# Kernel optimization log

Measured on AMD Instinct MI355X. Metric: run time of the kernel, lower is better.

The kernel has to match this reference:

```python
import jax, jax.numpy as jnp
import numpy as np

N = 100000      # total nodes across the batch of graphs
E = 1600000     # total edges (avg degree 16)
D = 128         # dim_drug (== num_feature here)
L = 3           # layer_drug
G = 2048        # number of graphs in the batch
BN_EPS = 1e-5


def setup_inputs() -> dict:
    key = jax.random.key(0)
    ks = jax.random.split(key, 10)
    x = jax.random.normal(ks[0], (N, D), dtype=jnp.float32)
    edge_index = jax.random.randint(ks[1], (2, E), 0, N, dtype=jnp.int64)
    batch = jnp.sort(jax.random.randint(ks[2], (N,), 0, G, dtype=jnp.int64))
    s = 0.05
    W1 = jax.random.normal(ks[3], (L, D, D), dtype=jnp.float32) * s
    b1 = jax.random.normal(ks[4], (L, D), dtype=jnp.float32) * s
    W2 = jax.random.normal(ks[5], (L, D, D), dtype=jnp.float32) * s
    b2 = jax.random.normal(ks[6], (L, D), dtype=jnp.float32) * s
    gamma = jnp.ones((L, D), dtype=jnp.float32)
    beta = jnp.zeros((L, D), dtype=jnp.float32)
    return {"x": x, "edge_index": edge_index, "batch": batch,
            "W1": W1, "b1": b1, "W2": W2, "b2": b2,
            "gamma": gamma, "beta": beta}


def reference(x, edge_index, batch, W1, b1, W2, b2, gamma, beta):
    src, dst = edge_index[0], edge_index[1]
    h = x
    layer_outs = []
    for i in range(L):
        # GINConv, eps=0: MLP( (1+eps)*h + sum_{j->i} h_j )
        agg = jax.ops.segment_sum(h[src], dst, num_segments=N)  # [N, D]
        m = agg + h
        m = jax.nn.relu(m @ W1[i] + b1[i]) @ W2[i] + b2[i]       # 2-layer MLP
        m = jax.nn.relu(m)                                        # F.relu after conv
        # BatchNorm1d (training mode: batch stats over node dim, biased var)
        mean = jnp.mean(m, axis=0)
        var = jnp.mean((m - mean) ** 2, axis=0)
        h = gamma[i] * (m - mean) * jax.lax.rsqrt(var + BN_EPS) + beta[i]
        layer_outs.append(h)
    node_rep = jnp.concatenate(layer_outs, axis=1)  # JK 'cat' -> [N, L*D]
    return jax.ops.segment_max(node_rep, batch, num_segments=G)  # [G, L*D]
```

## Files before the change

kernel.cpp:

```cpp
#include <hip/hip_runtime.h>
#include <stdint.h>

#define NN 100000
#define NE 1600000
#define DD 128
#define NL 3
#define NG 2048
#define BN_EPS 1e-5f
#define CAP 56
#define GSH 9
#define GSZ 512
#define NGRP 196
#define GBINCAP 9216
#define MAXSEG 16

typedef short s16x8 __attribute__((ext_vector_type(8)));
typedef float f32x4 __attribute__((ext_vector_type(4)));

__device__ __forceinline__ unsigned short f2bfu(float f) {
    union { float f; unsigned int i; } x; x.f = f;
    unsigned int r = x.i + 0x7fffu + ((x.i >> 16) & 1u);
    return (unsigned short)(r >> 16);
}
__device__ __forceinline__ float bfu2f(unsigned short u) {
    union { unsigned int i; float f; } x; x.i = ((unsigned int)u) << 16; return x.f;
}
__device__ __forceinline__ float uplo(unsigned int u) {
    union { unsigned int i; float f; } x; x.i = u << 16; return x.f;
}
__device__ __forceinline__ float uphi(unsigned int u) {
    union { unsigned int i; float f; } x; x.i = u & 0xffff0000u; return x.f;
}
__device__ __forceinline__ void add8(float* a, uint4 v) {
    a[0] += uplo(v.x); a[1] += uphi(v.x);
    a[2] += uplo(v.y); a[3] += uphi(v.y);
    a[4] += uplo(v.z); a[5] += uphi(v.z);
    a[6] += uplo(v.w); a[7] += uphi(v.w);
}
__device__ __forceinline__ unsigned int pack2(float a, float b) {
    return (unsigned int)f2bfu(a) | ((unsigned int)f2bfu(b) << 16);
}

__global__ __launch_bounds__(256) void k_cvt(
    const float* __restrict__ x, unsigned short* __restrict__ hb)
{
    int i = (blockIdx.x * 256 + threadIdx.x) * 4;
    if (i >= NN * DD) return;
    float4 v = *(const float4*)(x + i);
    ushort4 o;
    o.x = f2bfu(v.x); o.y = f2bfu(v.y); o.z = f2bfu(v.z); o.w = f2bfu(v.w);
    *(ushort4*)(hb + i) = o;
}

__global__ __launch_bounds__(256) void k_wtrans(
    const float* __restrict__ W1, const float* __restrict__ W2,
    unsigned short* __restrict__ Wt)
{
    int idx = blockIdx.x * 256 + threadIdx.x;
    if (idx >= 6 * DD * DD) return;
    int mat = idx >> 14;
    int r = idx & 16383;
    int n = r >> 7, k = r & 127;
    const float* src = (mat < 3) ? (W1 + mat * DD * DD) : (W2 + (mat - 3) * DD * DD);
    Wt[idx] = f2bfu(src[k * DD + n]);
}

__global__ __launch_bounds__(256) void k_bounds(
    const int* __restrict__ batch, int* __restrict__ start)
{
    int n = blockIdx.x * 256 + threadIdx.x;
    if (n >= NN) return;
    int bn = batch[n];
    bn = bn < 0 ? 0 : (bn > NG - 1 ? NG - 1 : bn);
    int bp;
    if (n == 0) bp = -1;
    else {
        bp = batch[n - 1];
        bp = bp < 0 ? 0 : (bp > NG - 1 ? NG - 1 : bp);
    }
    for (int g = bp + 1; g <= bn; ++g) start[g] = n;
    if (n == NN - 1) {
        for (int g = bn + 1; g <= NG; ++g) start[g] = NN;
    }
}

__global__ __launch_bounds__(256) void k_grp(
    const int* __restrict__ ei, int* __restrict__ gcnt,
    unsigned int* __restrict__ bins)
{
    __shared__ int hist[256];
    __shared__ int scn[256];
    __shared__ int exs[256];
    __shared__ int lofs[256];
    __shared__ int gbase[256];
    __shared__ unsigned int stage[4096];
    const int tid = threadIdx.x;
    hist[tid] = 0;
    __syncthreads();

    unsigned int pk[16];
    int gg[16];
    unsigned int vmask = 0;
    #pragma unroll
    for (int q = 0; q < 4; ++q) {
        long long e0 = (long long)blockIdx.x * 4096 + q * 1024 + tid * 4;
        if (e0 < NE) {
            const int* dp = ei + NE + e0;
            const int* sp = ei + e0;
            int dd_[4], ss_[4];
            dd_[0] = __builtin_nontemporal_load(dp + 0);
            dd_[1] = __builtin_nontemporal_load(dp + 1);
            dd_[2] = __builtin_nontemporal_load(dp + 2);
            dd_[3] = __builtin_nontemporal_load(dp + 3);
            ss_[0] = __builtin_nontemporal_load(sp + 0);
            ss_[1] = __builtin_nontemporal_load(sp + 1);
            ss_[2] = __builtin_nontemporal_load(sp + 2);
            ss_[3] = __builtin_nontemporal_load(sp + 3);
            #pragma unroll
            for (int i = 0; i < 4; ++i) {
                int dst = dd_[i], src = ss_[i];
                if ((unsigned)dst < NN && (unsigned)src < NN) {
                    int g = dst >> GSH;
                    int j = q * 4 + i;
                    pk[j] = ((unsigned)(dst & (GSZ - 1)) << 17) | (unsigned)src;
                    gg[j] = g;
                    atomicAdd(&hist[g], 1);
                    vmask |= 1u << j;
                }
            }
        }
    }
    __syncthreads();

    int v = hist[tid];
    scn[tid] = v;
    __syncthreads();
    #pragma unroll
    for (int off = 1; off < 256; off <<= 1) {
        int t = (tid >= off) ? scn[tid - off] : 0;
        __syncthreads();
        scn[tid] += t;
        __syncthreads();
    }
    int ex = scn[tid] - v;
    exs[tid] = ex;
    lofs[tid] = ex;
    if (tid < NGRP) {
        gbase[tid] = hist[tid] ? atomicAdd(&gcnt[tid], hist[tid]) : 0;
    }
    __syncthreads();

    #pragma unroll
    for (int j = 0; j < 16; ++j) {
        if (vmask & (1u << j)) {
            int p = atomicAdd(&lofs[gg[j]], 1);
            stage[p] = pk[j];
        }
    }
    __syncthreads();

    const int wave = tid >> 6, lane = tid & 63;
    for (int g = wave; g < NGRP; g += 4) {
        int len = hist[g];
        if (!len) continue;
        int gb = gbase[g], pb = exs[g];
        for (int k = lane; k < len; k += 64) {
            int o = gb + k;
            if (o < GBINCAP)
                bins[(long long)g * GBINCAP + o] = stage[pb + k];
        }
    }
}

__global__ __launch_bounds__(256, 1) void k_csr(
    const int* __restrict__ gcnt, const unsigned int* __restrict__ bins,
    int* __restrict__ cnt, int* __restrict__ csr)
{
    __shared__ int lcnt[GSZ];
    __shared__ int lcsr[GSZ * CAP];
    const int g = blockIdx.x;
    const int tid = threadIdx.x;
    for (int i = tid; i < GSZ; i += 256) lcnt[i] = 0;
    __syncthreads();

    int count = gcnt[g];
    count = count > GBINCAP ? GBINCAP : count;
    const unsigned int* bp = bins + (long long)g * GBINCAP;
    for (int e = tid * 4; e < count; e += 1024) {
        if (e + 4 <= count) {
            uint4 q4;
            q4.x = __builtin_nontemporal_load(bp + e + 0);
            q4.y = __builtin_nontemporal_load(bp + e + 1);
            q4.z = __builtin_nontemporal_load(bp + e + 2);
            q4.w = __builtin_nontemporal_load(bp + e + 3);
            unsigned int u[4] = {q4.x, q4.y, q4.z, q4.w};
            #pragma unroll
            for (int i = 0; i < 4; ++i) {
                int local = (int)(u[i] >> 17);
                int src = (int)(u[i] & 0x1FFFFu);
                int pos = atomicAdd(&lcnt[local], 1);
                if (pos < CAP) lcsr[local * CAP + pos] = src;
            }
        } else {
            for (int i = e; i < count; ++i) {
                unsigned int u = bp[i];
                int local = (int)(u >> 17);
                int src = (int)(u & 0x1FFFFu);
                int pos = atomicAdd(&lcnt[local], 1);
                if (pos < CAP) lcsr[local * CAP + pos] = src;
            }
        }
    }
    __syncthreads();

    const int nbase = g << GSH;
    int nmax = NN - nbase;
    nmax = nmax > GSZ ? GSZ : nmax;
    for (int i = tid; i < nmax; i += 256) cnt[nbase + i] = lcnt[i];
    const int tot = nmax * CAP;
    int* dstp = csr + (long long)nbase * CAP;
    for (int i = tid * 4; i < tot; i += 1024)
        *(int4*)(dstp + i) = *(const int4*)(&lcsr[i]);
}

template <bool L0>
__global__ __launch_bounds__(256) void k_agg(
    const unsigned short* __restrict__ hb, const int* __restrict__ cnt,
    const int* __restrict__ csr, unsigned short* __restrict__ aggf,
    const float* __restrict__ stats_prev, const float* __restrict__ gamma_prev,
    const float* __restrict__ beta_prev)
{
    const int node = blockIdx.x * 16 + (threadIdx.x >> 4);
    const int lane = threadIdx.x & 15;
    if (node >= NN) return;
    float af[8], cf[8];
    if (L0) {
        #pragma unroll
        for (int j = 0; j < 8; ++j) { af[j] = 1.0f; cf[j] = 0.0f; }
    } else {
        const float inv_n = 1.0f / (float)NN;
        #pragma unroll
        for (int j = 0; j < 8; ++j) {
            int d = lane * 8 + j;
            float mean = stats_prev[d] * inv_n;
            float var = stats_prev[DD + d] * inv_n - mean * mean;
            float inv = rsqrtf(fmaxf(var, 0.f) + BN_EPS);
            af[j] = gamma_prev[d] * inv;
            cf[j] = beta_prev[d] - mean * af[j];
        }
    }
    int deg = cnt[node];
    deg = deg > CAP ? CAP : deg;
    const int* bkt = csr + node * CAP;
    const unsigned short* base = hb + lane * 8;
    float acc[8];
    {
        uint4 v = *(const uint4*)(base + (long long)node * DD);
        acc[0] = uplo(v.x); acc[1] = uphi(v.x);
        acc[2] = uplo(v.y); acc[3] = uphi(v.y);
        acc[4] = uplo(v.z); acc[5] = uphi(v.z);
        acc[6] = uplo(v.w); acc[7] = uphi(v.w);
    }
    int e = 0;
    for (; e + 8 <= deg; e += 8) {
        int4 i0 = *(const int4*)(bkt + e);
        int4 i1 = *(const int4*)(bkt + e + 4);
        uint4 v0 = *(const uint4*)(base + (long long)i0.x * DD);
        uint4 v1 = *(const uint4*)(base + (long long)i0.y * DD);
        uint4 v2 = *(const uint4*)(base + (long long)i0.z * DD);
        uint4 v3 = *(const uint4*)(base + (long long)i0.w * DD);
        uint4 v4 = *(const uint4*)(base + (long long)i1.x * DD);
        uint4 v5 = *(const uint4*)(base + (long long)i1.y * DD);
        uint4 v6 = *(const uint4*)(base + (long long)i1.z * DD);
        uint4 v7 = *(const uint4*)(base + (long long)i1.w * DD);
        add8(acc, v0); add8(acc, v1); add8(acc, v2); add8(acc, v3);
        add8(acc, v4); add8(acc, v5); add8(acc, v6); add8(acc, v7);
    }
    for (; e + 4 <= deg; e += 4) {
        int4 i0 = *(const int4*)(bkt + e);
        uint4 v0 = *(const uint4*)(base + (long long)i0.x * DD);
        uint4 v1 = *(const uint4*)(base + (long long)i0.y * DD);
        uint4 v2 = *(const uint4*)(base + (long long)i0.z * DD);
        uint4 v3 = *(const uint4*)(base + (long long)i0.w * DD);
        add8(acc, v0); add8(acc, v1); add8(acc, v2); add8(acc, v3);
    }
    for (; e < deg; ++e) {
        uint4 v = *(const uint4*)(base + (long long)bkt[e] * DD);
        add8(acc, v);
    }
    if (!L0) {
        float dp1 = (float)(deg + 1);
        #pragma unroll
        for (int j = 0; j < 8; ++j)
            acc[j] = af[j] * acc[j] + cf[j] * dp1;
    }
    uint4 o;
    o.x = pack2(acc[0], acc[1]);
    o.y = pack2(acc[2], acc[3]);
    o.z = pack2(acc[4], acc[5]);
    o.w = pack2(acc[6], acc[7]);
    *(uint4*)(aggf + (long long)node * DD + lane * 8) = o;
}

template <bool WRH>
__global__ __launch_bounds__(256, 2) void k_mlp(
    const unsigned short* __restrict__ aggf, unsigned short* __restrict__ hout,
    const unsigned short* __restrict__ W1t, const float* __restrict__ b1,
    const unsigned short* __restrict__ W2t, const float* __restrict__ b2,
    float* __restrict__ stats, const int* __restrict__ batch,
    unsigned int* __restrict__ gmxl, unsigned int* __restrict__ gmnl)
{
    __shared__ unsigned short lA[128 * 136];
    __shared__ unsigned short lW[128 * 136];
    __shared__ float sSum[4][128];
    __shared__ float sSq[4][128];
    __shared__ int sB[128];
    const int tid = threadIdx.x;
    const int row0 = blockIdx.x * 128;

    if (tid < 128) {
        int row = row0 + tid;
        int b = batch[row < NN ? row : NN - 1];
        b = b < 0 ? 0 : (b > NG - 1 ? NG - 1 : b);
        sB[tid] = b;
    }
    #pragma unroll
    for (int it = 0; it < 8; ++it) {
        int eidx = (it * 256 + tid) * 8;
        int r = eidx >> 7, c = eidx & 127;
        *(uint4*)(&lW[r * 136 + c]) = *(const uint4*)(W1t + eidx);
    }
    {
        int col8 = tid & 15, rr = tid >> 4;
        #pragma unroll
        for (int it = 0; it < 8; ++it) {
            int r = rr + it * 16;
            int grow = row0 + r;
            uint4 v;
            if (grow < NN) {
                v = *(const uint4*)(aggf + (long long)grow * DD + col8 * 8);
            } else {
                v.x = v.y = v.z = v.w = 0;
            }
            *(uint4*)(&lA[r * 136 + col8 * 8]) = v;
        }
    }
    __syncthreads();

    const int wave = tid >> 6, lane = tid & 63;
    const int quad = lane >> 4, m16 = lane & 15;

    f32x4 acc[2][8] = {};
    #pragma unroll
    for (int k0 = 0; k0 < 128; k0 += 32) {
        const int kk = k0 + quad * 8;
        s16x8 a0 = *(const s16x8*)(&lA[(wave * 32 + m16) * 136 + kk]);
        s16x8 a1 = *(const s16x8*)(&lA[(wave * 32 + 16 + m16) * 136 + kk]);
        #pragma unroll
        for (int ct = 0; ct < 8; ++ct) {
            s16x8 bf = *(const s16x8*)(&lW[(ct * 16 + m16) * 136 + kk]);
            acc[0][ct] = __builtin_amdgcn_mfma_f32_16x16x32_bf16(a0, bf, acc[0][ct], 0, 0, 0);
            acc[1][ct] = __builtin_amdgcn_mfma_f32_16x16x32_bf16(a1, bf, acc[1][ct], 0, 0, 0);
        }
    }
    __syncthreads();

    #pragma unroll
    for (int rt = 0; rt < 2; ++rt) {
        #pragma unroll
        for (int ct = 0; ct < 8; ++ct) {
            int col = ct * 16 + m16;
            float b = b1[col];
            #pragma unroll
            for (int r = 0; r < 4; ++r) {
                int lrow = wave * 32 + rt * 16 + quad * 4 + r;
                lA[lrow * 136 + col] = f2bfu(fmaxf(acc[rt][ct][r] + b, 0.0f));
            }
        }
    }
    #pragma unroll
    for (int it = 0; it < 8; ++it) {
        int eidx = (it * 256 + tid) * 8;
        int r = eidx >> 7, c = eidx & 127;
        *(uint4*)(&lW[r * 136 + c]) = *(const uint4*)(W2t + eidx);
    }
    __syncthreads();

    #pragma unroll
    for (int rt = 0; rt < 2; ++rt)
        #pragma unroll
        for (int ct = 0; ct < 8; ++ct)
            acc[rt][ct] = f32x4{0.f, 0.f, 0.f, 0.f};
    #pragma unroll
    for (int k0 = 0; k0 < 128; k0 += 32) {
        const int kk = k0 + quad * 8;
        s16x8 a0 = *(const s16x8*)(&lA[(wave * 32 + m16) * 136 + kk]);
        s16x8 a1 = *(const s16x8*)(&lA[(wave * 32 + 16 + m16) * 136 + kk]);
        #pragma unroll
        for (int ct = 0; ct < 8; ++ct) {
            s16x8 bf = *(const s16x8*)(&lW[(ct * 16 + m16) * 136 + kk]);
            acc[0][ct] = __builtin_amdgcn_mfma_f32_16x16x32_bf16(a0, bf, acc[0][ct], 0, 0, 0);
            acc[1][ct] = __builtin_amdgcn_mfma_f32_16x16x32_bf16(a1, bf, acc[1][ct], 0, 0, 0);
        }
    }
    __syncthreads();

    unsigned int* lseg = (unsigned int*)lA;
    for (int i = tid; i < 2048; i += 256) {
        lseg[i] = 0u;
        lseg[i + 2048] = 0x7f7f7f7fu;
    }
    __syncthreads();

    const int g_first = sB[0];
    int nvalid = NN - row0; nvalid = nvalid > 128 ? 128 : nvalid;
    const int nseg = sB[nvalid - 1] - g_first + 1;
    const bool ldsok = (nseg <= MAXSEG);

    float csum[8] = {}, csq[8] = {};
    #pragma unroll
    for (int rt = 0; rt < 2; ++rt) {
        int lbase = wave * 32 + rt * 16 + quad * 4;
        int rbase = row0 + lbase;
        #pragma unroll
        for (int ct = 0; ct < 8; ++ct) {
            int col = ct * 16 + m16;
            float b = b2[col];
            int sprev = -1;
            float rmx = 0.f, rmn = 0.f;
            #pragma unroll
            for (int r = 0; r < 4; ++r) {
                int row = rbase + r;
                if (row < NN) {
                    float v = fmaxf(acc[rt][ct][r] + b, 0.0f);
                    if (WRH) hout[(long long)row * DD + col] = f2bfu(v);
                    csum[ct] += v;
                    csq[ct] += v * v;
                    int s = sB[lbase + r] - g_first;
                    if (s == sprev) {
                        rmx = fmaxf(rmx, v); rmn = fminf(rmn, v);
                    } else {
                        if (sprev >= 0) {
                            if (ldsok) {
                                atomicMax(&lseg[sprev * 128 + col], __float_as_uint(rmx));
                                atomicMin(&lseg[2048 + sprev * 128 + col], __float_as_uint(rmn));
                            } else {
                                atomicMax(&gmxl[(g_first + sprev) * DD + col], __float_as_uint(rmx));
                                atomicMin(&gmnl[(g_first + sprev) * DD + col], __float_as_uint(rmn));
                            }
                        }
                        sprev = s; rmx = v; rmn = v;
                    }
                }
            }
            if (sprev >= 0) {
                if (ldsok) {
                    atomicMax(&lseg[sprev * 128 + col], __float_as_uint(rmx));
                    atomicMin(&lseg[2048 + sprev * 128 + col], __float_as_uint(rmn));
                } else {
                    atomicMax(&gmxl[(g_first + sprev) * DD + col], __float_as_uint(rmx));
                    atomicMin(&gmnl[(g_first + sprev) * DD + col], __float_as_uint(rmn));
                }
            }
        }
    }
    #pragma unroll
    for (int ct = 0; ct < 8; ++ct) {
        csum[ct] += __shfl_xor(csum[ct], 16);
        csum[ct] += __shfl_xor(csum[ct], 32);
        csq[ct]  += __shfl_xor(csq[ct], 16);
        csq[ct]  += __shfl_xor(csq[ct], 32);
    }
    if (quad == 0) {
        #pragma unroll
        for (int ct = 0; ct < 8; ++ct) {
            int col = ct * 16 + m16;
            sSum[wave][col] = csum[ct];
            sSq[wave][col] = csq[ct];
        }
    }
    __syncthreads();
    if (ldsok) {
        for (int i = tid; i < nseg * 128; i += 256) {
            int g = g_first + (i >> 7), col = i & 127;
            unsigned int um = lseg[i], un = lseg[2048 + i];
            if (um) atomicMax(&gmxl[g * DD + col], um);
            if (un != 0x7f7f7f7fu) atomicMin(&gmnl[g * DD + col], un);
        }
    }
    if (tid < 128) {
        float s = sSum[0][tid] + sSum[1][tid] + sSum[2][tid] + sSum[3][tid];
        float q = sSq[0][tid] + sSq[1][tid] + sSq[2][tid] + sSq[3][tid];
        atomicAdd(&stats[tid], s);
        atomicAdd(&stats[DD + tid], q);
    }
}

__global__ __launch_bounds__(256) void k_out(
    const float* __restrict__ stats, const float* __restrict__ gamma,
    const float* __restrict__ beta, const int* __restrict__ start,
    const unsigned int* __restrict__ gmx, const unsigned int* __restrict__ gmn,
    float* __restrict__ out)
{
    int idx = blockIdx.x * 256 + threadIdx.x;
    if (idx >= NL * NG * DD) return;
    int l = idx / (NG * DD);
    int rem = idx - l * NG * DD;
    int g = rem >> 7;
    int d = rem & 127;
    const float inv_n = 1.0f / (float)NN;
    float mean = stats[l * 256 + d] * inv_n;
    float var = stats[l * 256 + DD + d] * inv_n - mean * mean;
    float inv = rsqrtf(fmaxf(var, 0.f) + BN_EPS);
    float a = gamma[l * DD + d] * inv;
    float c = beta[l * DD + d] - mean * a;
    int n0 = start[g], n1 = start[g + 1];
    float res = 0.f;
    if (n1 > n0) {
        float mx = __uint_as_float(gmx[(l * NG + g) * DD + d]);
        float mn = __uint_as_float(gmn[(l * NG + g) * DD + d]);
        res = (a >= 0.f) ? fmaf(a, mx, c) : fmaf(a, mn, c);
    }
    out[(long long)g * (NL * DD) + l * DD + d] = res;
}

extern "C" void kernel_launch(void* const* d_in, const int* in_sizes, int n_in,
                              void* d_out, int out_size, void* d_ws, size_t ws_size,
                              hipStream_t stream) {
    const float* x     = (const float*)d_in[0];
    const int*   ei    = (const int*)d_in[1];
    const int*   batch = (const int*)d_in[2];
    const float* W1    = (const float*)d_in[3];
    const float* b1    = (const float*)d_in[4];
    const float* W2    = (const float*)d_in[5];
    const float* b2    = (const float*)d_in[6];
    const float* gamma = (const float*)d_in[7];
    const float* beta  = (const float*)d_in[8];
    float* out = (float*)d_out;
    unsigned short* aggf = (unsigned short*)d_in[0];
    unsigned int*   bins = (unsigned int*)((char*)d_in[0] + 25600000);
    unsigned int*   gmx  = (unsigned int*)((char*)d_in[0] + 32825344);
    unsigned int*   gmn  = (unsigned int*)((char*)d_in[0] + 35971072);

    char* p = (char*)d_ws;
    float*          stats = (float*)p;
    int*            gcnt  = (int*)(p + 3072);
    int*            cnt   = (int*)(p + 4096);
    int*            start = (int*)(p + 405504);
    unsigned short* Wt    = (unsigned short*)(p + 417792);
    int*            csr   = (int*)(p + 614400);
    unsigned short* hb    = (unsigned short*)(p + 23014400);

    hipMemsetAsync(p, 0, 404096, stream);
    k_cvt<<<(NN * DD / 4 + 255) / 256, 256, 0, stream>>>(x, hb);
    hipMemsetAsync(gmx, 0x00, NL * NG * DD * 4, stream);
    hipMemsetAsync(gmn, 0x7f, NL * NG * DD * 4, stream);
    k_wtrans<<<(6 * DD * DD + 255) / 256, 256, 0, stream>>>(W1, W2, Wt);
    k_bounds<<<(NN + 255) / 256, 256, 0, stream>>>(batch, start);
    k_grp<<<(NE + 4095) / 4096, 256, 0, stream>>>(ei, gcnt, bins);
    k_csr<<<NGRP, 256, 0, stream>>>(gcnt, bins, cnt, csr);

    const int nblk = (NN + 127) / 128;
    for (int l = 0; l < NL; ++l) {
        float* stats_l = stats + l * 256;
        unsigned int* gmxl = gmx + l * NG * DD;
        unsigned int* gmnl = gmn + l * NG * DD;
        if (l == 0)
            k_agg<true><<<(NN + 15) / 16, 256, 0, stream>>>(
                hb, cnt, csr, aggf, nullptr, nullptr, nullptr);
        else
            k_agg<false><<<(NN + 15) / 16, 256, 0, stream>>>(
                hb, cnt, csr, aggf,
                stats + (l - 1) * 256, gamma + (l - 1) * DD, beta + (l - 1) * DD);
        if (l < NL - 1)
            k_mlp<true><<<nblk, 256, 0, stream>>>(
                aggf, hb, Wt + l * DD * DD, b1 + l * DD,
                Wt + (3 + l) * DD * DD, b2 + l * DD,
                stats_l, batch, gmxl, gmnl);
        else
            k_mlp<false><<<nblk, 256, 0, stream>>>(
                aggf, hb, Wt + l * DD * DD, b1 + l * DD,
                Wt + (3 + l) * DD * DD, b2 + l * DD,
                stats_l, batch, gmxl, gmnl);
    }
    k_out<<<(NL * NG * DD + 255) / 256, 256, 0, stream>>>(
        stats, gamma, beta, start, gmx, gmn, out);
}
```

Before: 502.2 us.

## Batch gathers in fixed 16-edge chunks and shrink MLP tiles to 64 rows

The aggregation kernel now issues neighbour loads in fixed blocks of 16. Out-of-range slots load the node's own row, and that padding is subtracted afterwards, so every load in a chunk is independent and there are no remainder loops. The BN affine coefficients are now computed after the gather instead of before it. The MLP kernel processes 64 rows per block with 4 waves of 16 rows and a smaller LDS footprint (132 stride, reused LDS for segments and stats), and raises the occupancy hint to 3 blocks per CU. This doubles the number of blocks and W1/W2 reloads per row, and padding adds redundant self-row loads.

```diff
diff --git a/kernel.cpp b/kernel.cpp
--- a/kernel.cpp
+++ b/kernel.cpp
@@ -12,7 +12,7 @@
 #define GSZ 512
 #define NGRP 196
 #define GBINCAP 9216
-#define MAXSEG 16
+#define MAXSEG 8
 
 typedef short s16x8 __attribute__((ext_vector_type(8)));
 typedef float f32x4 __attribute__((ext_vector_type(4)));
@@ -233,66 +233,57 @@
     const int node = blockIdx.x * 16 + (threadIdx.x >> 4);
     const int lane = threadIdx.x & 15;
     if (node >= NN) return;
-    float af[8], cf[8];
-    if (L0) {
-        #pragma unroll
-        for (int j = 0; j < 8; ++j) { af[j] = 1.0f; cf[j] = 0.0f; }
-    } else {
+    int deg = cnt[node];
+    deg = deg > CAP ? CAP : deg;
+    const int* bkt = csr + node * CAP;
+    const unsigned short* base = hb + lane * 8;
+    float self8[8], acc[8];
+    {
+        uint4 v = *(const uint4*)(base + (long long)node * DD);
+        self8[0] = uplo(v.x); self8[1] = uphi(v.x);
+        self8[2] = uplo(v.y); self8[3] = uphi(v.y);
+        self8[4] = uplo(v.z); self8[5] = uphi(v.z);
+        self8[6] = uplo(v.w); self8[7] = uphi(v.w);
+        #pragma unroll
+        for (int j = 0; j < 8; ++j) acc[j] = self8[j];
+    }
+    const int nb = (deg + 15) >> 4;
+    for (int b = 0; b < nb; ++b) {
+        const int e0 = b * 16;
+        int4 i0 = *(const int4*)(bkt + e0);
+        int4 i1 = *(const int4*)(bkt + e0 + 4);
+        int4 i2 = *(const int4*)(bkt + e0 + 8);
+        int4 i3 = *(const int4*)(bkt + e0 + 12);
+        int idx[16] = {i0.x, i0.y, i0.z, i0.w, i1.x, i1.y, i1.z, i1.w,
+                       i2.x, i2.y, i2.z, i2.w, i3.x, i3.y, i3.z, i3.w};
+        uint4 v[16];
+        #pragma unroll
+        for (int i = 0; i < 16; ++i) {
+            int id = (e0 + i < deg) ? idx[i] : node;
+            v[i] = *(const uint4*)(base + (long long)id * DD);
+        }
+        #pragma unroll
+        for (int i = 0; i < 16; ++i) add8(acc, v[i]);
+    }
+    int pad = nb * 16 - deg;
+    if (pad) {
+        float pf = (float)pad;
+        #pragma unroll
+        for (int j = 0; j < 8; ++j) acc[j] = fmaf(-pf, self8[j], acc[j]);
+    }
+    if (!L0) {
         const float inv_n = 1.0f / (float)NN;
+        const float dp1 = (float)(deg + 1);
         #pragma unroll
         for (int j = 0; j < 8; ++j) {
             int d = lane * 8 + j;
             float mean = stats_prev[d] * inv_n;
             float var = stats_prev[DD + d] * inv_n - mean * mean;
             float inv = rsqrtf(fmaxf(var, 0.f) + BN_EPS);
-            af[j] = gamma_prev[d] * inv;
-            cf[j] = beta_prev[d] - mean * af[j];
-        }
-    }
-    int deg = cnt[node];
-    deg = deg > CAP ? CAP : deg;
-    const int* bkt = csr + node * CAP;
-    const unsigned short* base = hb + lane * 8;
-    float acc[8];
-    {
-        uint4 v = *(const uint4*)(base + (long long)node * DD);
-        acc[0] = uplo(v.x); acc[1] = uphi(v.x);
-        acc[2] = uplo(v.y); acc[3] = uphi(v.y);
-        acc[4] = uplo(v.z); acc[5] = uphi(v.z);
-        acc[6] = uplo(v.w); acc[7] = uphi(v.w);
-    }
-    int e = 0;
-    for (; e + 8 <= deg; e += 8) {
-        int4 i0 = *(const int4*)(bkt + e);
-        int4 i1 = *(const int4*)(bkt + e + 4);
-        uint4 v0 = *(const uint4*)(base + (long long)i0.x * DD);
-        uint4 v1 = *(const uint4*)(base + (long long)i0.y * DD);
-        uint4 v2 = *(const uint4*)(base + (long long)i0.z * DD);
-        uint4 v3 = *(const uint4*)(base + (long long)i0.w * DD);
-        uint4 v4 = *(const uint4*)(base + (long long)i1.x * DD);
-        uint4 v5 = *(const uint4*)(base + (long long)i1.y * DD);
-        uint4 v6 = *(const uint4*)(base + (long long)i1.z * DD);
-        uint4 v7 = *(const uint4*)(base + (long long)i1.w * DD);
-        add8(acc, v0); add8(acc, v1); add8(acc, v2); add8(acc, v3);
-        add8(acc, v4); add8(acc, v5); add8(acc, v6); add8(acc, v7);
-    }
-    for (; e + 4 <= deg; e += 4) {
-        int4 i0 = *(const int4*)(bkt + e);
-        uint4 v0 = *(const uint4*)(base + (long long)i0.x * DD);
-        uint4 v1 = *(const uint4*)(base + (long long)i0.y * DD);
-        uint4 v2 = *(const uint4*)(base + (long long)i0.z * DD);
-        uint4 v3 = *(const uint4*)(base + (long long)i0.w * DD);
-        add8(acc, v0); add8(acc, v1); add8(acc, v2); add8(acc, v3);
-    }
-    for (; e < deg; ++e) {
-        uint4 v = *(const uint4*)(base + (long long)bkt[e] * DD);
-        add8(acc, v);
-    }
-    if (!L0) {
-        float dp1 = (float)(deg + 1);
-        #pragma unroll
-        for (int j = 0; j < 8; ++j)
-            acc[j] = af[j] * acc[j] + cf[j] * dp1;
+            float a = gamma_prev[d] * inv;
+            float c = beta_prev[d] - mean * a;
+            acc[j] = a * acc[j] + c * dp1;
+        }
     }
     uint4 o;
     o.x = pack2(acc[0], acc[1]);
@@ -303,22 +294,20 @@
 }
 
 template <bool WRH>
-__global__ __launch_bounds__(256, 2) void k_mlp(
+__global__ __launch_bounds__(256, 3) void k_mlp(
     const unsigned short* __restrict__ aggf, unsigned short* __restrict__ hout,
     const unsigned short* __restrict__ W1t, const float* __restrict__ b1,
     const unsigned short* __restrict__ W2t, const float* __restrict__ b2,
     float* __restrict__ stats, const int* __restrict__ batch,
     unsigned int* __restrict__ gmxl, unsigned int* __restrict__ gmnl)
 {
-    __shared__ unsigned short lA[128 * 136];
-    __shared__ unsigned short lW[128 * 136];
-    __shared__ float sSum[4][128];
-    __shared__ float sSq[4][128];
-    __shared__ int sB[128];
+    __shared__ unsigned short lA[64 * 132];
+    __shared__ unsigned short lW[128 * 132];
+    __shared__ int sB[64];
     const int tid = threadIdx.x;
-    const int row0 = blockIdx.x * 128;
-
-    if (tid < 128) {
+    const int row0 = blockIdx.x * 64;
+
+    if (tid < 64) {
         int row = row0 + tid;
         int b = batch[row < NN ? row : NN - 1];
         b = b < 0 ? 0 : (b > NG - 1 ? NG - 1 : b);
@@ -328,12 +317,12 @@
     for (int it = 0; it < 8; ++it) {
         int eidx = (it * 256 + tid) * 8;
         int r = eidx >> 7, c = eidx & 127;
-        *(uint4*)(&lW[r * 136 + c]) = *(const uint4*)(W1t + eidx);
+        *(uint4*)(&lW[r * 132 + c]) = *(const uint4*)(W1t + eidx);
     }
     {
         int col8 = tid & 15, rr = tid >> 4;
         #pragma unroll
-        for (int it = 0; it < 8; ++it) {
+        for (int it = 0; it < 4; ++it) {
             int r = rr + it * 16;
             int grow = row0 + r;
             uint4 v;
@@ -342,86 +331,79 @@
             } else {
                 v.x = v.y = v.z = v.w = 0;
             }
-            *(uint4*)(&lA[r * 136 + col8 * 8]) = v;
+            *(uint4*)(&lA[r * 132 + col8 * 8]) = v;
         }
     }
     __syncthreads();
 
     const int wave = tid >> 6, lane = tid & 63;
     const int quad = lane >> 4, m16 = lane & 15;
-
-    f32x4 acc[2][8] = {};
+    const int wrow = wave * 16;
+
+    f32x4 acc[8] = {};
     #pragma unroll
     for (int k0 = 0; k0 < 128; k0 += 32) {
         const int kk = k0 + quad * 8;
-        s16x8 a0 = *(const s16x8*)(&lA[(wave * 32 + m16) * 136 + kk]);
-        s16x8 a1 = *(const s16x8*)(&lA[(wave * 32 + 16 + m16) * 136 + kk]);
+        s16x8 a0 = *(const s16x8*)(&lA[(wrow + m16) * 132 + kk]);
         #pragma unroll
         for (int ct = 0; ct < 8; ++ct) {
-            s16x8 bf = *(const s16x8*)(&lW[(ct * 16 + m16) * 136 + kk]);
-            acc[0][ct] = __builtin_amdgcn_mfma_f32_16x16x32_bf16(a0, bf, acc[0][ct], 0, 0, 0);
-            acc[1][ct] = __builtin_amdgcn_mfma_f32_16x16x32_bf16(a1, bf, acc[1][ct], 0, 0, 0);
-        }
-    }
-    __syncthreads();
-
-    #pragma unroll
-    for (int rt = 0; rt < 2; ++rt) {
-        #pragma unroll
-        for (int ct = 0; ct < 8; ++ct) {
-            int col = ct * 16 + m16;
-            float b = b1[col];
-            #pragma unroll
-            for (int r = 0; r < 4; ++r) {
-                int lrow = wave * 32 + rt * 16 + quad * 4 + r;
-                lA[lrow * 136 + col] = f2bfu(fmaxf(acc[rt][ct][r] + b, 0.0f));
-            }
+            s16x8 bf = *(const s16x8*)(&lW[(ct * 16 + m16) * 132 + kk]);
+            acc[ct] = __builtin_amdgcn_mfma_f32_16x16x32_bf16(a0, bf, acc[ct], 0, 0, 0);
+        }
+    }
+    __syncthreads();
+
+    #pragma unroll
+    for (int ct = 0; ct < 8; ++ct) {
+        int col = ct * 16 + m16;
+        float b = b1[col];
+        #pragma unroll
+        for (int r = 0; r < 4; ++r) {
+            int lrow = wrow + quad * 4 + r;
+            lA[lrow * 132 + col] = f2bfu(fmaxf(acc[ct][r] + b, 0.0f));
         }
     }
     #pragma unroll
     for (int it = 0; it < 8; ++it) {
         int eidx = (it * 256 + tid) * 8;
         int r = eidx >> 7, c = eidx & 127;
-        *(uint4*)(&lW[r * 136 + c]) = *(const uint4*)(W2t + eidx);
-    }
-    __syncthreads();
-
-    #pragma unroll
-    for (int rt = 0; rt < 2; ++rt)
-        #pragma unroll
-        for (int ct = 0; ct < 8; ++ct)
-            acc[rt][ct] = f32x4{0.f, 0.f, 0.f, 0.f};
+        *(uint4*)(&lW[r * 132 + c]) = *(const uint4*)(W2t + eidx);
+    }
+    __syncthreads();
+
+    #pragma unroll
+    for (int ct = 0; ct < 8; ++ct) acc[ct] = f32x4{0.f, 0.f, 0.f, 0.f};
     #pragma unroll
     for (int k0 = 0; k0 < 128; k0 += 32) {
         const int kk = k0 + quad * 8;
-        s16x8 a0 = *(const s16x8*)(&lA[(wave * 32 + m16) * 136 + kk]);
-        s16x8 a1 = *(const s16x8*)(&lA[(wave * 32 + 16 + m16) * 136 + kk]);
+        s16x8 a0 = *(const s16x8*)(&lA[(wrow + m16) * 132 + kk]);
         #pragma unroll
         for (int ct = 0; ct < 8; ++ct) {
-            s16x8 bf = *(const s16x8*)(&lW[(ct * 16 + m16) * 136 + kk]);
-            acc[0][ct] = __builtin_amdgcn_mfma_f32_16x16x32_bf16(a0, bf, acc[0][ct], 0, 0, 0);
-            acc[1][ct] = __builtin_amdgcn_mfma_f32_16x16x32_bf16(a1, bf, acc[1][ct], 0, 0, 0);
-        }
-    }
-    __syncthreads();
-
-    unsigned int* lseg = (unsigned int*)lA;
-    for (int i = tid; i < 2048; i += 256) {
-        lseg[i] = 0u;
-        lseg[i + 2048] = 0x7f7f7f7fu;
+            s16x8 bf = *(const s16x8*)(&lW[(ct * 16 + m16) * 132 + kk]);
+            acc[ct] = __builtin_amdgcn_mfma_f32_16x16x32_bf16(a0, bf, acc[ct], 0, 0, 0);
+        }
+    }
+    __syncthreads();
+
+    unsigned int* lsegMax = (unsigned int*)lA;
+    unsigned int* lsegMin = lsegMax + MAXSEG * 128;
+    float* sSum = (float*)(lsegMin + MAXSEG * 128);
+    float* sSq  = sSum + 4 * 128;
+    for (int i = tid; i < MAXSEG * 128; i += 256) {
+        lsegMax[i] = 0u;
+        lsegMin[i] = 0x7f7f7f7fu;
     }
     __syncthreads();
 
     const int g_first = sB[0];
-    int nvalid = NN - row0; nvalid = nvalid > 128 ? 128 : nvalid;
+    int nvalid = NN - row0; nvalid = nvalid > 64 ? 64 : nvalid;
     const int nseg = sB[nvalid - 1] - g_first + 1;
     const bool ldsok = (nseg <= MAXSEG);
 
     float csum[8] = {}, csq[8] = {};
-    #pragma unroll
-    for (int rt = 0; rt < 2; ++rt) {
-        int lbase = wave * 32 + rt * 16 + quad * 4;
-        int rbase = row0 + lbase;
+    {
+        const int lbase = wrow + quad * 4;
+        const int rbase = row0 + lbase;
         #pragma unroll
         for (int ct = 0; ct < 8; ++ct) {
             int col = ct * 16 + m16;
@@ -432,7 +414,7 @@
             for (int r = 0; r < 4; ++r) {
                 int row = rbase + r;
                 if (row < NN) {
-                    float v = fmaxf(acc[rt][ct][r] + b, 0.0f);
+                    float v = fmaxf(acc[ct][r] + b, 0.0f);
                     if (WRH) hout[(long long)row * DD + col] = f2bfu(v);
                     csum[ct] += v;
                     csq[ct] += v * v;
@@ -442,8 +424,8 @@
                     } else {
                         if (sprev >= 0) {
                             if (ldsok) {
-                                atomicMax(&lseg[sprev * 128 + col], __float_as_uint(rmx));
-                                atomicMin(&lseg[2048 + sprev * 128 + col], __float_as_uint(rmn));
+                                atomicMax(&lsegMax[sprev * 128 + col], __float_as_uint(rmx));
+                                atomicMin(&lsegMin[sprev * 128 + col], __float_as_uint(rmn));
                             } else {
                                 atomicMax(&gmxl[(g_first + sprev) * DD + col], __float_as_uint(rmx));
                                 atomicMin(&gmnl[(g_first + sprev) * DD + col], __float_as_uint(rmn));
@@ -455,8 +437,8 @@
             }
             if (sprev >= 0) {
                 if (ldsok) {
-                    atomicMax(&lseg[sprev * 128 + col], __float_as_uint(rmx));
-                    atomicMin(&lseg[2048 + sprev * 128 + col], __float_as_uint(rmn));
+                    atomicMax(&lsegMax[sprev * 128 + col], __float_as_uint(rmx));
+                    atomicMin(&lsegMin[sprev * 128 + col], __float_as_uint(rmn));
                 } else {
                     atomicMax(&gmxl[(g_first + sprev) * DD + col], __float_as_uint(rmx));
                     atomicMin(&gmnl[(g_first + sprev) * DD + col], __float_as_uint(rmn));
@@ -475,22 +457,22 @@
         #pragma unroll
         for (int ct = 0; ct < 8; ++ct) {
             int col = ct * 16 + m16;
-            sSum[wave][col] = csum[ct];
-            sSq[wave][col] = csq[ct];
+            sSum[wave * 128 + col] = csum[ct];
+            sSq[wave * 128 + col] = csq[ct];
         }
     }
     __syncthreads();
     if (ldsok) {
         for (int i = tid; i < nseg * 128; i += 256) {
             int g = g_first + (i >> 7), col = i & 127;
-            unsigned int um = lseg[i], un = lseg[2048 + i];
+            unsigned int um = lsegMax[i], un = lsegMin[i];
             if (um) atomicMax(&gmxl[g * DD + col], um);
             if (un != 0x7f7f7f7fu) atomicMin(&gmnl[g * DD + col], un);
         }
     }
     if (tid < 128) {
-        float s = sSum[0][tid] + sSum[1][tid] + sSum[2][tid] + sSum[3][tid];
-        float q = sSq[0][tid] + sSq[1][tid] + sSq[2][tid] + sSq[3][tid];
+        float s = sSum[tid] + sSum[128 + tid] + sSum[256 + tid] + sSum[384 + tid];
+        float q = sSq[tid] + sSq[128 + tid] + sSq[256 + tid] + sSq[384 + tid];
         atomicAdd(&stats[tid], s);
         atomicAdd(&stats[DD + tid], q);
     }
@@ -560,7 +542,7 @@
     k_grp<<<(NE + 4095) / 4096, 256, 0, stream>>>(ei, gcnt, bins);
     k_csr<<<NGRP, 256, 0, stream>>>(gcnt, bins, cnt, csr);
 
-    const int nblk = (NN + 127) / 128;
+    const int nblk = (NN + 63) / 64;
     for (int l = 0; l < NL; ++l) {
         float* stats_l = stats + l * 256;
         unsigned int* gmxl = gmx + l * NG * DD;
```

Result: slower. 520.7 us (+3.7%).
